# Kernel optimization log

Measured on AMD Instinct MI355X. Metric: run time of the kernel, lower is better.

## Reference

```python
import jax, jax.numpy as jnp
import numpy as np

EMBED = 1024
HEADS = 16
HEAD_DIM = EMBED // HEADS
SEQ = 2048
BATCH = 2


def setup_inputs() -> dict:
    key = jax.random.key(0)
    ks = jax.random.split(key, 5)
    s = 1.0 / np.sqrt(EMBED)
    return {
        "x": jax.random.normal(ks[0], (BATCH, SEQ, EMBED), jnp.float32),
        "W_qkv": jax.random.uniform(ks[1], (EMBED, 3 * EMBED), jnp.float32, -s, s),
        "b_qkv": jax.random.uniform(ks[2], (3 * EMBED,), jnp.float32, -s, s),
        "W_out": jax.random.uniform(ks[3], (EMBED, EMBED), jnp.float32, -s, s),
        "b_out": jax.random.uniform(ks[4], (EMBED,), jnp.float32, -s, s),
    }


def reference(x, W_qkv, b_qkv, W_out, b_out):
    B, S, E = x.shape
    qkv = x @ W_qkv + b_qkv                      # [B,S,3E]
    q, k, v = jnp.split(qkv, 3, axis=-1)
    # [B,S,E] -> [B,H,S,D]
    def heads(t):
        return t.reshape(B, S, HEADS, HEAD_DIM).transpose(0, 2, 1, 3)
    q, k, v = heads(q), heads(k), heads(v)
    scores = jnp.einsum("bhid,bhjd->bhij", q, k) / np.sqrt(HEAD_DIM)  # [B,H,S,S]
    causal = jnp.tril(jnp.ones((S, S), bool))
    scores = jnp.where(causal[None, None], scores, -jnp.inf)
    probs = jax.nn.softmax(scores, axis=-1)
    out = jnp.einsum("bhij,bhjd->bhid", probs, v)  # [B,H,S,D]
    out = out.transpose(0, 2, 1, 3).reshape(B, S, E)
    return out @ W_out + b_out
```

## Files before the change

### kernel.cpp

```cpp
#include <hip/hip_runtime.h>
#include <hip/hip_bf16.h>
#include <cstdint>
#include <cstddef>


typedef unsigned short u16;
typedef __attribute__((ext_vector_type(8))) short short8;
typedef __attribute__((ext_vector_type(4))) short short4v;
typedef __attribute__((ext_vector_type(4))) float floatx4;

#define MFMA16(a, b, c) __builtin_amdgcn_mfma_f32_16x16x32_bf16((a), (b), (c), 0, 0, 0)

#if __has_builtin(__builtin_amdgcn_mfma_f32_16x16x16_bf16)
#define PV_MFMA(a, b, c) __builtin_amdgcn_mfma_f32_16x16x16_bf16((a), (b), (c), 0, 0, 0)
#elif __has_builtin(__builtin_amdgcn_mfma_f32_16x16x16bf16_1k)
#define PV_MFMA(a, b, c) __builtin_amdgcn_mfma_f32_16x16x16bf16_1k((a), (b), (c), 0, 0, 0)
#else
static __device__ __forceinline__ floatx4 pv_mfma_asm(short4v a, short4v b, floatx4 c) {
    asm volatile("v_mfma_f32_16x16x16_bf16 %0, %1, %2, %0" : "+v"(c) : "v"(a), "v"(b));
    return c;
}
#define PV_MFMA(a, b, c) pv_mfma_asm((a), (b), (c))
#endif

#if __has_builtin(__builtin_amdgcn_exp2f)
#define EXP2(x) __builtin_amdgcn_exp2f(x)
#else
#define EXP2(x) exp2f(x)
#endif

#define QSCALE 0.18033688011f

static __device__ __forceinline__ u16 f2b(float f) {
    union { float f; uint32_t u; } v; v.f = f;
    return (u16)((v.u + 0x7fffu + ((v.u >> 16) & 1u)) >> 16);
}

static __device__ __forceinline__ uint32_t pkbf(float lo, float hi) {
    union { float f; uint32_t u; } a, b; a.f = lo; b.f = hi;
    return __builtin_amdgcn_perm(b.u + 0x8000u, a.u + 0x8000u, 0x07060302u);
}

static __device__ __forceinline__ void async_cp16(const u16* g, u16* lds_wave_base) {
    __builtin_amdgcn_global_load_lds((__attribute__((address_space(1))) void*)g,
                                     (__attribute__((address_space(3))) void*)lds_wave_base,
                                     16, 0, 0);
}


__global__ __launch_bounds__(256) void k_f32_to_bf16(const float* __restrict__ src,
                                                     u16* __restrict__ dst, int n8) {
    int g = blockIdx.x * 256 + threadIdx.x;
    if (g >= n8) return;
    const float4* s = (const float4*)src + (size_t)g * 2;
    float4 f0 = s[0];
    float4 f1 = s[1];
    alignas(16) u16 r[8] = {f2b(f0.x), f2b(f0.y), f2b(f0.z), f2b(f0.w),
                            f2b(f1.x), f2b(f1.y), f2b(f1.z), f2b(f1.w)};
    *(uint4*)(dst + (size_t)g * 8) = *(const uint4*)r;
}

__global__ __launch_bounds__(256) void k_transpose_to_bf16(const float* __restrict__ src,
                                                           u16* __restrict__ dst,
                                                           int R, int C) {
    __shared__ float t[32][33];
    int tx = threadIdx.x, ty = threadIdx.y;
    int c0 = blockIdx.x * 32, r0 = blockIdx.y * 32;
#pragma unroll
    for (int i = 0; i < 4; ++i)
        t[ty + i * 8][tx] = src[(size_t)(r0 + ty + i * 8) * C + c0 + tx];
    __syncthreads();
#pragma unroll
    for (int i = 0; i < 4; ++i)
        dst[(size_t)(c0 + ty + i * 8) * R + r0 + tx] = f2b(t[tx][ty + i * 8]);
}


__global__ __launch_bounds__(256) void k_qkv_gemm(const u16* __restrict__ A,
                                                  const u16* __restrict__ Bt,
                                                  const float* __restrict__ bias,
                                                  u16* __restrict__ Qb,
                                                  u16* __restrict__ Kb,
                                                  u16* __restrict__ Vtb) {
    __shared__ __align__(16) u16 As[128 * 64];
    __shared__ __align__(16) u16 Bs[128 * 64];
    int tid = threadIdx.x;
    int w = tid >> 6, lane = tid & 63, quad = lane >> 4, l16 = lane & 15;
    int wm = w >> 1, wn = w & 1;
    int m0 = blockIdx.y * 128, n0 = blockIdx.x * 128;
    int wb8 = (tid & ~63) * 8;
    floatx4 acc[4][4] = {};

    for (int kt = 0; kt < 16; ++kt) {
#pragma unroll
        for (int i = 0; i < 4; ++i) {
            int f = i * 256 + tid;
            int r = f >> 3, c = (f & 7) ^ (r & 7);
            async_cp16(&A[(size_t)(m0 + r) * 1024 + kt * 64 + c * 8], &As[i * 2048 + wb8]);
        }
#pragma unroll
        for (int i = 0; i < 4; ++i) {
            int f = i * 256 + tid;
            int r = f >> 3, c = (f & 7) ^ (r & 7);
            async_cp16(&Bt[(size_t)(n0 + r) * 1024 + kt * 64 + c * 8], &Bs[i * 2048 + wb8]);
        }
        __syncthreads();
#pragma unroll
        for (int ks = 0; ks < 2; ++ks) {
            short8 af[4], bf[4];
            int sw = l16 & 7;
#pragma unroll
            for (int mt = 0; mt < 4; ++mt)
                af[mt] = *(const short8*)&As[((wm * 64 + mt * 16 + l16) * 8 + ((ks * 4 + quad) ^ sw)) * 8];
#pragma unroll
            for (int nt = 0; nt < 4; ++nt)
                bf[nt] = *(const short8*)&Bs[((wn * 64 + nt * 16 + l16) * 8 + ((ks * 4 + quad) ^ sw)) * 8];
#pragma unroll
            for (int mt = 0; mt < 4; ++mt)
#pragma unroll
                for (int nt = 0; nt < 4; ++nt)
                    acc[mt][nt] = MFMA16(af[mt], bf[nt], acc[mt][nt]);
        }
        __syncthreads();
    }

    int region = n0 >> 10;
    if (region == 2) {
#pragma unroll
        for (int mt = 0; mt < 4; ++mt)
#pragma unroll
            for (int nt = 0; nt < 4; ++nt) {
                int n_abs = n0 + wn * 64 + nt * 16 + l16;
                int e = n_abs & 1023, h = e >> 6, d = e & 63;
                float vb = bias[n_abs];
                int mrow = m0 + wm * 64 + mt * 16 + quad * 4;
                int b = mrow >> 11, s0 = mrow & 2047;
                uint2 val;
                val.x = pkbf(acc[mt][nt][0] + vb, acc[mt][nt][1] + vb);
                val.y = pkbf(acc[mt][nt][2] + vb, acc[mt][nt][3] + vb);
                *(uint2*)&Vtb[((size_t)(b * 16 + h) * 64 + d) * 2048 + s0] = val;
            }
    } else {
        u16* dst = region == 0 ? Qb : Kb;
        float scl = region == 0 ? QSCALE : 1.0f;
#pragma unroll
        for (int mt = 0; mt < 4; ++mt)
#pragma unroll
            for (int nt = 0; nt < 4; ++nt)
#pragma unroll
                for (int r = 0; r < 4; ++r) {
                    int m_abs = m0 + wm * 64 + mt * 16 + quad * 4 + r;
                    int n_abs = n0 + wn * 64 + nt * 16 + l16;
                    float val = (acc[mt][nt][r] + bias[n_abs]) * scl;
                    int e = n_abs & 1023, h = e >> 6, d = e & 63;
                    int b = m_abs >> 11, s = m_abs & 2047;
                    dst[((size_t)(b * 16 + h) * 2048 + s) * 64 + d] = f2b(val);
                }
    }
}


__global__ __launch_bounds__(256) void k_out_gemm(const u16* __restrict__ A,
                                                  const u16* __restrict__ Bt,
                                                  const float* __restrict__ bias,
                                                  float* __restrict__ out) {
    __shared__ __align__(16) u16 As[64 * 64];
    __shared__ __align__(16) u16 Bs[128 * 64];
    int tid = threadIdx.x;
    int w = tid >> 6, lane = tid & 63, quad = lane >> 4, l16 = lane & 15;
    int wm = w >> 1, wn = w & 1;
    int m0 = blockIdx.y * 64, n0 = blockIdx.x * 128;
    int wb8 = (tid & ~63) * 8;
    floatx4 acc[2][4] = {};

    for (int kt = 0; kt < 16; ++kt) {
#pragma unroll
        for (int i = 0; i < 2; ++i) {
            int f = i * 256 + tid;
            int r = f >> 3, c = (f & 7) ^ (r & 7);
            async_cp16(&A[(size_t)(m0 + r) * 1024 + kt * 64 + c * 8], &As[i * 2048 + wb8]);
        }
#pragma unroll
        for (int i = 0; i < 4; ++i) {
            int f = i * 256 + tid;
            int r = f >> 3, c = (f & 7) ^ (r & 7);
            async_cp16(&Bt[(size_t)(n0 + r) * 1024 + kt * 64 + c * 8], &Bs[i * 2048 + wb8]);
        }
        __syncthreads();
#pragma unroll
        for (int ks = 0; ks < 2; ++ks) {
            short8 af[2], bf[4];
            int sw = l16 & 7;
#pragma unroll
            for (int mt = 0; mt < 2; ++mt)
                af[mt] = *(const short8*)&As[((wm * 32 + mt * 16 + l16) * 8 + ((ks * 4 + quad) ^ sw)) * 8];
#pragma unroll
            for (int nt = 0; nt < 4; ++nt)
                bf[nt] = *(const short8*)&Bs[((wn * 64 + nt * 16 + l16) * 8 + ((ks * 4 + quad) ^ sw)) * 8];
#pragma unroll
            for (int mt = 0; mt < 2; ++mt)
#pragma unroll
                for (int nt = 0; nt < 4; ++nt)
                    acc[mt][nt] = MFMA16(af[mt], bf[nt], acc[mt][nt]);
        }
        __syncthreads();
    }

#pragma unroll
    for (int mt = 0; mt < 2; ++mt)
#pragma unroll
        for (int nt = 0; nt < 4; ++nt)
#pragma unroll
            for (int r = 0; r < 4; ++r) {
                int m_abs = m0 + wm * 32 + mt * 16 + quad * 4 + r;
                int n_abs = n0 + wn * 64 + nt * 16 + l16;
                out[(size_t)m_abs * 1024 + n_abs] = acc[mt][nt][r] + bias[n_abs];
            }
}


__global__ __launch_bounds__(256, 2) void k_attn(const u16* __restrict__ Qb,
                                                 const u16* __restrict__ Kb,
                                                 const u16* __restrict__ Vtb,
                                                 u16* __restrict__ attnb) {
    __shared__ __align__(16) u16 KV[4][2][4096];
    int tid = threadIdx.x;
    int w = tid >> 6, lane = tid & 63, quad = lane >> 4, l16 = lane & 15;
    int L = blockIdx.x;
    int bh = ((L & 7) << 2) | ((L >> 3) & 3);
    int idx = (L >> 5) & 15;
    int pr = idx < 8 ? idx : 23 - idx;
    int qta = pr, qtb = 31 - pr;
    const u16* Qp = Qb + (size_t)bh * 131072;
    const u16* Kp = Kb + (size_t)bh * 131072;
    const u16* Vp = Vtb + (size_t)bh * 131072;
    int b = bh >> 4, h = bh & 15;

    int r0 = tid >> 3, c0 = ((tid & 7) ^ (r0 & 7)) * 8;
    int f1 = 256 + tid;
    int r1 = f1 >> 3, c1 = ((f1 & 7) ^ (r1 & 7)) * 8;
    int kOff0 = r0 * 64 + c0, kOff1 = r1 * 64 + c1;
    int vOff0 = r0 * 2048 + c0, vOff1 = r1 * 2048 + c1;
    int wb = (tid & ~63) * 8;

    int qrowa = qta * 64 + w * 16 + l16;
    int qrowb = qtb * 64 + w * 16 + l16;
    short8 qa0 = *(const short8*)&Qp[(size_t)qrowa * 64 + quad * 8];
    short8 qa1 = *(const short8*)&Qp[(size_t)qrowa * 64 + 32 + quad * 8];
    short8 qb0 = *(const short8*)&Qp[(size_t)qrowb * 64 + quad * 8];
    short8 qb1 = *(const short8*)&Qp[(size_t)qrowb * 64 + 32 + quad * 8];

    int n = qtb + 1;

    auto stage = [&](int j) {
        u16* Ks = (u16*)KV[j & 3][0];
        u16* Vs = (u16*)KV[j & 3][1];
        const u16* kp = Kp + (size_t)j * 4096;
        const u16* vp = Vp + (size_t)j * 64;
        async_cp16(kp + kOff0, Ks + wb);
        async_cp16(kp + kOff1, Ks + 2048 + wb);
        async_cp16(vp + vOff0, Vs + wb);
        async_cp16(vp + vOff1, Vs + 2048 + wb);
    };

    floatx4 accA[4] = {}, accB[4] = {};
    float ma = -__builtin_inff(), la = 0.f;
    float mb = -__builtin_inff(), lb = 0.f;
    int sw = l16 & 7;

    stage(0); stage(1); stage(2);

    for (int kt = 0; kt < n; ++kt) {
        asm volatile("s_waitcnt vmcnt(8)" ::: "memory");
        asm volatile("s_barrier" ::: "memory");
        {
            int jn = kt + 3;
            stage(jn < n ? jn : n - 1);
        }
        const u16* Ks = (const u16*)KV[kt & 3][0];
        const u16* Vs = (const u16*)KV[kt & 3][1];

        short8 kfa[4], kfb[4];
#pragma unroll
        for (int nt = 0; nt < 4; ++nt) {
            int rb = (nt * 16 + l16) * 8;
            kfa[nt] = *(const short8*)&Ks[(rb + (quad ^ sw)) * 8];
            kfb[nt] = *(const short8*)&Ks[(rb + ((4 + quad) ^ sw)) * 8];
        }
        short4v vf[4][4];
#pragma unroll
        for (int dt = 0; dt < 4; ++dt) {
            const char* rowb = (const char*)Vs + (dt * 16 + l16) * 128 + (quad & 1) * 8;
#pragma unroll
            for (int nt = 0; nt < 4; ++nt) {
                int chunk = nt * 2 + (quad >> 1);
                vf[nt][dt] = *(const short4v*)(rowb + ((chunk ^ sw) * 16));
            }
        }

        auto tile_step = [&](short8 qf0, short8 qf1, int qt_this, float& mr, float& lr,
                             floatx4* accO) {
            floatx4 sa[4] = {};
#pragma unroll
            for (int nt = 0; nt < 4; ++nt) {
                sa[nt] = MFMA16(kfa[nt], qf0, sa[nt]);
                sa[nt] = MFMA16(kfb[nt], qf1, sa[nt]);
            }
            if (kt == qt_this) {
                int q_abs = qt_this * 64 + w * 16 + l16;
#pragma unroll
                for (int nt = 0; nt < 4; ++nt)
#pragma unroll
                    for (int r = 0; r < 4; ++r)
                        if (kt * 64 + nt * 16 + quad * 4 + r > q_abs)
                            sa[nt][r] = -__builtin_inff();
            }
            float v = sa[0][0];
#pragma unroll
            for (int nt = 0; nt < 4; ++nt)
#pragma unroll
                for (int r = 0; r < 4; ++r) v = fmaxf(v, sa[nt][r]);
            v = fmaxf(v, __shfl_xor(v, 16));
            v = fmaxf(v, __shfl_xor(v, 32));
            float m_new = fmaxf(mr, v);
            float alpha = EXP2(mr - m_new);
            float p[4][4];
            float rs = 0.f;
#pragma unroll
            for (int nt = 0; nt < 4; ++nt)
#pragma unroll
                for (int r = 0; r < 4; ++r) {
                    float e = EXP2(sa[nt][r] - m_new);
                    p[nt][r] = e;
                    rs += e;
                }
            rs += __shfl_xor(rs, 16);
            rs += __shfl_xor(rs, 32);
            lr = lr * alpha + rs;
            mr = m_new;
#pragma unroll
            for (int dt = 0; dt < 4; ++dt)
#pragma unroll
                for (int r = 0; r < 4; ++r) accO[dt][r] *= alpha;
#pragma unroll
            for (int nt = 0; nt < 4; ++nt) {
                union { uint2 u; short4v s; } pf;
                pf.u.x = pkbf(p[nt][0], p[nt][1]);
                pf.u.y = pkbf(p[nt][2], p[nt][3]);
#pragma unroll
                for (int dt = 0; dt < 4; ++dt)
                    accO[dt] = PV_MFMA(vf[nt][dt], pf.s, accO[dt]);
            }
        };

        tile_step(qb0, qb1, qtb, mb, lb, accB);
        if (kt <= qta) tile_step(qa0, qa1, qta, ma, la, accA);
    }

    auto epilogue = [&](int qt_this, float lr, const floatx4* accO) {
        int q_abs = qt_this * 64 + w * 16 + l16;
        float inv = 1.f / lr;
        size_t base = ((size_t)(b * 2048 + q_abs)) * 1024 + h * 64;
#pragma unroll
        for (int dt = 0; dt < 4; ++dt) {
            uint2 val;
            val.x = pkbf(accO[dt][0] * inv, accO[dt][1] * inv);
            val.y = pkbf(accO[dt][2] * inv, accO[dt][3] * inv);
            *(uint2*)&attnb[base + dt * 16 + quad * 4] = val;
        }
    };
    epilogue(qta, la, accA);
    epilogue(qtb, lb, accB);
}


extern "C" void kernel_launch(void* const* d_in, const int* in_sizes, int n_in,
                              void* d_out, int out_size, void* d_ws, size_t ws_size,
                              hipStream_t stream) {
    const float* x     = (const float*)d_in[0];
    const float* W_qkv = (const float*)d_in[1];
    const float* b_qkv = (const float*)d_in[2];
    const float* W_out = (const float*)d_in[3];
    const float* b_out = (const float*)d_in[4];
    float* out = (float*)d_out;

    char* p = (char*)d_ws;
    u16* xb    = (u16*)p; p += (size_t)4096 * 1024 * 2;
    u16* wqkvT = (u16*)p; p += (size_t)3072 * 1024 * 2;
    u16* woutT = (u16*)p; p += (size_t)1024 * 1024 * 2;
    u16* Qb    = (u16*)p; p += (size_t)32 * 2048 * 64 * 2;
    u16* Kb    = (u16*)p; p += (size_t)32 * 2048 * 64 * 2;
    u16* Vtb   = (u16*)p; p += (size_t)32 * 64 * 2048 * 2;
    u16* attnb = xb;

    k_f32_to_bf16<<<(4096 * 1024 / 8) / 256, 256, 0, stream>>>(x, xb, 4096 * 1024 / 8);
    dim3 tb(32, 8);
    k_transpose_to_bf16<<<dim3(3072 / 32, 1024 / 32), tb, 0, stream>>>(W_qkv, wqkvT, 1024, 3072);
    k_transpose_to_bf16<<<dim3(1024 / 32, 1024 / 32), tb, 0, stream>>>(W_out, woutT, 1024, 1024);
    k_qkv_gemm<<<dim3(24, 32), 256, 0, stream>>>(xb, wqkvT, b_qkv, Qb, Kb, Vtb);
    k_attn<<<512, 256, 0, stream>>>(Qb, Kb, Vtb, attnb);
    k_out_gemm<<<dim3(8, 64), 256, 0, stream>>>(attnb, woutT, b_out, out);
}
```

Baseline: 189.8 us.

## Triple-buffer GEMM K loops with async LDS loads and merge prep kernels

Both GEMMs now use a three-slot LDS ring with a K tile of 32, issuing global-to-LDS copies two stages ahead. They drop the double __syncthreads per iteration in favour of a vmcnt wait plus a single barrier. The three preparation launches (x conversion and two weight transposes) are merged into one k_prep kernel, and x conversion uses the cheaper pkbf packing. This is meant to hide global load latency behind MFMA work and cut launch overhead, at the cost of removing the XOR LDS swizzle, which may bring bank conflicts, and of relying on hand-written waitcnt counts being correct.

```diff
diff --git a/kernel.cpp b/kernel.cpp
--- a/kernel.cpp
+++ b/kernel.cpp
@@ -48,24 +48,35 @@
 }
 
 
-__global__ __launch_bounds__(256) void k_f32_to_bf16(const float* __restrict__ src,
-                                                     u16* __restrict__ dst, int n8) {
-    int g = blockIdx.x * 256 + threadIdx.x;
-    if (g >= n8) return;
-    const float4* s = (const float4*)src + (size_t)g * 2;
-    float4 f0 = s[0];
-    float4 f1 = s[1];
-    alignas(16) u16 r[8] = {f2b(f0.x), f2b(f0.y), f2b(f0.z), f2b(f0.w),
-                            f2b(f1.x), f2b(f1.y), f2b(f1.z), f2b(f1.w)};
-    *(uint4*)(dst + (size_t)g * 8) = *(const uint4*)r;
-}
-
-__global__ __launch_bounds__(256) void k_transpose_to_bf16(const float* __restrict__ src,
-                                                           u16* __restrict__ dst,
-                                                           int R, int C) {
+__global__ __launch_bounds__(256) void k_prep(const float* __restrict__ x,
+                                              const float* __restrict__ Wq,
+                                              const float* __restrict__ Wo,
+                                              u16* __restrict__ xb,
+                                              u16* __restrict__ wqkvT,
+                                              u16* __restrict__ woutT) {
+    int bx = blockIdx.x, tid = threadIdx.x;
+    if (bx < 2048) {
+        int g = bx * 256 + tid;
+        const float4* s = (const float4*)x + (size_t)g * 2;
+        float4 f0 = s[0], f1 = s[1];
+        uint4 r;
+        r.x = pkbf(f0.x, f0.y);
+        r.y = pkbf(f0.z, f0.w);
+        r.z = pkbf(f1.x, f1.y);
+        r.w = pkbf(f1.z, f1.w);
+        *(uint4*)(xb + (size_t)g * 8) = r;
+        return;
+    }
     __shared__ float t[32][33];
-    int tx = threadIdx.x, ty = threadIdx.y;
-    int c0 = blockIdx.x * 32, r0 = blockIdx.y * 32;
+    const float* src;
+    u16* dst;
+    int R, C, b;
+    if (bx < 5120) { b = bx - 2048; src = Wq; dst = wqkvT; R = 1024; C = 3072; }
+    else           { b = bx - 5120; src = Wo; dst = woutT; R = 1024; C = 1024; }
+    int nbx = C >> 5;
+    int yq = b / nbx, xq = b - yq * nbx;
+    int c0 = xq * 32, r0 = yq * 32;
+    int tx = tid & 31, ty = tid >> 5;
 #pragma unroll
     for (int i = 0; i < 4; ++i)
         t[ty + i * 8][tx] = src[(size_t)(r0 + ty + i * 8) * C + c0 + tx];
@@ -76,52 +87,57 @@
 }
 
 
-__global__ __launch_bounds__(256) void k_qkv_gemm(const u16* __restrict__ A,
-                                                  const u16* __restrict__ Bt,
-                                                  const float* __restrict__ bias,
-                                                  u16* __restrict__ Qb,
-                                                  u16* __restrict__ Kb,
-                                                  u16* __restrict__ Vtb) {
-    __shared__ __align__(16) u16 As[128 * 64];
-    __shared__ __align__(16) u16 Bs[128 * 64];
+__global__ __launch_bounds__(256, 3) void k_qkv_gemm(const u16* __restrict__ A,
+                                                     const u16* __restrict__ Bt,
+                                                     const float* __restrict__ bias,
+                                                     u16* __restrict__ Qb,
+                                                     u16* __restrict__ Kb,
+                                                     u16* __restrict__ Vtb) {
+    __shared__ __align__(16) u16 As[3][128 * 32];
+    __shared__ __align__(16) u16 Bs[3][128 * 32];
     int tid = threadIdx.x;
     int w = tid >> 6, lane = tid & 63, quad = lane >> 4, l16 = lane & 15;
     int wm = w >> 1, wn = w & 1;
     int m0 = blockIdx.y * 128, n0 = blockIdx.x * 128;
-    int wb8 = (tid & ~63) * 8;
+    int wb = (tid & ~63) * 8;
+
+    int ra0 = tid >> 2, ca0 = (tid & 3) * 8;
+    int ra1 = (256 + tid) >> 2, ca1 = (tid & 3) * 8;
+    const u16* A0 = &A[(size_t)(m0 + ra0) * 1024 + ca0];
+    const u16* A1 = &A[(size_t)(m0 + ra1) * 1024 + ca1];
+    const u16* B0 = &Bt[(size_t)(n0 + ra0) * 1024 + ca0];
+    const u16* B1 = &Bt[(size_t)(n0 + ra1) * 1024 + ca1];
+
+    auto stage = [&](int src_kt, int slot) {
+        int ko = src_kt * 32;
+        async_cp16(A0 + ko, &As[slot][wb]);
+        async_cp16(A1 + ko, &As[slot][2048 + wb]);
+        async_cp16(B0 + ko, &Bs[slot][wb]);
+        async_cp16(B1 + ko, &Bs[slot][2048 + wb]);
+    };
+
     floatx4 acc[4][4] = {};
-
-    for (int kt = 0; kt < 16; ++kt) {
-#pragma unroll
-        for (int i = 0; i < 4; ++i) {
-            int f = i * 256 + tid;
-            int r = f >> 3, c = (f & 7) ^ (r & 7);
-            async_cp16(&A[(size_t)(m0 + r) * 1024 + kt * 64 + c * 8], &As[i * 2048 + wb8]);
-        }
-#pragma unroll
-        for (int i = 0; i < 4; ++i) {
-            int f = i * 256 + tid;
-            int r = f >> 3, c = (f & 7) ^ (r & 7);
-            async_cp16(&Bt[(size_t)(n0 + r) * 1024 + kt * 64 + c * 8], &Bs[i * 2048 + wb8]);
-        }
-        __syncthreads();
-#pragma unroll
-        for (int ks = 0; ks < 2; ++ks) {
-            short8 af[4], bf[4];
-            int sw = l16 & 7;
-#pragma unroll
-            for (int mt = 0; mt < 4; ++mt)
-                af[mt] = *(const short8*)&As[((wm * 64 + mt * 16 + l16) * 8 + ((ks * 4 + quad) ^ sw)) * 8];
+    stage(0, 0);
+    stage(1, 1);
+
+    for (int kt = 0; kt < 32; ++kt) {
+        asm volatile("s_waitcnt vmcnt(4)" ::: "memory");
+        asm volatile("s_barrier" ::: "memory");
+        int jn = kt + 2;
+        stage(jn < 32 ? jn : 31, jn % 3);
+        int s = kt % 3;
+        short8 af[4], bf[4];
+#pragma unroll
+        for (int mt = 0; mt < 4; ++mt)
+            af[mt] = *(const short8*)&As[s][(wm * 64 + mt * 16 + l16) * 32 + quad * 8];
+#pragma unroll
+        for (int nt = 0; nt < 4; ++nt)
+            bf[nt] = *(const short8*)&Bs[s][(wn * 64 + nt * 16 + l16) * 32 + quad * 8];
+#pragma unroll
+        for (int mt = 0; mt < 4; ++mt)
 #pragma unroll
             for (int nt = 0; nt < 4; ++nt)
-                bf[nt] = *(const short8*)&Bs[((wn * 64 + nt * 16 + l16) * 8 + ((ks * 4 + quad) ^ sw)) * 8];
-#pragma unroll
-            for (int mt = 0; mt < 4; ++mt)
-#pragma unroll
-                for (int nt = 0; nt < 4; ++nt)
-                    acc[mt][nt] = MFMA16(af[mt], bf[nt], acc[mt][nt]);
-        }
-        __syncthreads();
+                acc[mt][nt] = MFMA16(af[mt], bf[nt], acc[mt][nt]);
     }
 
     int region = n0 >> 10;
@@ -160,50 +176,53 @@
 }
 
 
-__global__ __launch_bounds__(256) void k_out_gemm(const u16* __restrict__ A,
-                                                  const u16* __restrict__ Bt,
-                                                  const float* __restrict__ bias,
-                                                  float* __restrict__ out) {
-    __shared__ __align__(16) u16 As[64 * 64];
-    __shared__ __align__(16) u16 Bs[128 * 64];
+__global__ __launch_bounds__(256, 4) void k_out_gemm(const u16* __restrict__ A,
+                                                     const u16* __restrict__ Bt,
+                                                     const float* __restrict__ bias,
+                                                     float* __restrict__ out) {
+    __shared__ __align__(16) u16 As[3][64 * 32];
+    __shared__ __align__(16) u16 Bs[3][128 * 32];
     int tid = threadIdx.x;
     int w = tid >> 6, lane = tid & 63, quad = lane >> 4, l16 = lane & 15;
     int wm = w >> 1, wn = w & 1;
     int m0 = blockIdx.y * 64, n0 = blockIdx.x * 128;
-    int wb8 = (tid & ~63) * 8;
+    int wb = (tid & ~63) * 8;
+
+    int ra0 = tid >> 2, ca0 = (tid & 3) * 8;
+    int ra1 = (256 + tid) >> 2;
+    const u16* A0 = &A[(size_t)(m0 + ra0) * 1024 + ca0];
+    const u16* B0 = &Bt[(size_t)(n0 + ra0) * 1024 + ca0];
+    const u16* B1 = &Bt[(size_t)(n0 + ra1) * 1024 + ca0];
+
+    auto stage = [&](int src_kt, int slot) {
+        int ko = src_kt * 32;
+        async_cp16(A0 + ko, &As[slot][wb]);
+        async_cp16(B0 + ko, &Bs[slot][wb]);
+        async_cp16(B1 + ko, &Bs[slot][2048 + wb]);
+    };
+
     floatx4 acc[2][4] = {};
-
-    for (int kt = 0; kt < 16; ++kt) {
-#pragma unroll
-        for (int i = 0; i < 2; ++i) {
-            int f = i * 256 + tid;
-            int r = f >> 3, c = (f & 7) ^ (r & 7);
-            async_cp16(&A[(size_t)(m0 + r) * 1024 + kt * 64 + c * 8], &As[i * 2048 + wb8]);
-        }
-#pragma unroll
-        for (int i = 0; i < 4; ++i) {
-            int f = i * 256 + tid;
-            int r = f >> 3, c = (f & 7) ^ (r & 7);
-            async_cp16(&Bt[(size_t)(n0 + r) * 1024 + kt * 64 + c * 8], &Bs[i * 2048 + wb8]);
-        }
-        __syncthreads();
-#pragma unroll
-        for (int ks = 0; ks < 2; ++ks) {
-            short8 af[2], bf[4];
-            int sw = l16 & 7;
-#pragma unroll
-            for (int mt = 0; mt < 2; ++mt)
-                af[mt] = *(const short8*)&As[((wm * 32 + mt * 16 + l16) * 8 + ((ks * 4 + quad) ^ sw)) * 8];
+    stage(0, 0);
+    stage(1, 1);
+
+    for (int kt = 0; kt < 32; ++kt) {
+        asm volatile("s_waitcnt vmcnt(3)" ::: "memory");
+        asm volatile("s_barrier" ::: "memory");
+        int jn = kt + 2;
+        stage(jn < 32 ? jn : 31, jn % 3);
+        int s = kt % 3;
+        short8 af[2], bf[4];
+#pragma unroll
+        for (int mt = 0; mt < 2; ++mt)
+            af[mt] = *(const short8*)&As[s][(wm * 32 + mt * 16 + l16) * 32 + quad * 8];
+#pragma unroll
+        for (int nt = 0; nt < 4; ++nt)
+            bf[nt] = *(const short8*)&Bs[s][(wn * 64 + nt * 16 + l16) * 32 + quad * 8];
+#pragma unroll
+        for (int mt = 0; mt < 2; ++mt)
 #pragma unroll
             for (int nt = 0; nt < 4; ++nt)
-                bf[nt] = *(const short8*)&Bs[((wn * 64 + nt * 16 + l16) * 8 + ((ks * 4 + quad) ^ sw)) * 8];
-#pragma unroll
-            for (int mt = 0; mt < 2; ++mt)
-#pragma unroll
-                for (int nt = 0; nt < 4; ++nt)
-                    acc[mt][nt] = MFMA16(af[mt], bf[nt], acc[mt][nt]);
-        }
-        __syncthreads();
+                acc[mt][nt] = MFMA16(af[mt], bf[nt], acc[mt][nt]);
     }
 
 #pragma unroll
@@ -393,10 +412,7 @@
     u16* Vtb   = (u16*)p; p += (size_t)32 * 64 * 2048 * 2;
     u16* attnb = xb;
 
-    k_f32_to_bf16<<<(4096 * 1024 / 8) / 256, 256, 0, stream>>>(x, xb, 4096 * 1024 / 8);
-    dim3 tb(32, 8);
-    k_transpose_to_bf16<<<dim3(3072 / 32, 1024 / 32), tb, 0, stream>>>(W_qkv, wqkvT, 1024, 3072);
-    k_transpose_to_bf16<<<dim3(1024 / 32, 1024 / 32), tb, 0, stream>>>(W_out, woutT, 1024, 1024);
+    k_prep<<<6144, 256, 0, stream>>>(x, W_qkv, W_out, xb, wqkvT, woutT);
     k_qkv_gemm<<<dim3(24, 32), 256, 0, stream>>>(xb, wqkvT, b_qkv, Qb, Kb, Vtb);
     k_attn<<<512, 256, 0, stream>>>(Qb, Kb, Vtb, attnb);
     k_out_gemm<<<dim3(8, 64), 256, 0, stream>>>(attnb, woutT, b_out, out);
```

After: 179.8 us. 1.06x faster.
